# Kernel tuning notes

Measured on AMD Instinct MI355X. Metric: run time of the kernel, lower is better.

Reference implementation:

```python
import jax, jax.numpy as jnp
import numpy as np

NTIME = 20      # number of time blocks
V = 128         # vehicle_num per time block
F_OUT = 128     # out_features (== in_features here)
ALPHA = 0.2     # LeakyReLU negative slope
NEG = -9e15     # mask fill value used by the torch module


def setup_inputs() -> dict:
    key = jax.random.key(0)
    k1, k2, k3, k4 = jax.random.split(key, 4)
    h = jax.random.normal(k1, (NTIME * V, F_OUT), dtype=jnp.float32)
    # binary adjacency mask, broadcast over the feature dim like the torch code
    adj = jax.random.randint(k2, (V, V, 1), 0, 2).astype(jnp.float32)
    share_weight = jax.random.normal(k3, (F_OUT, F_OUT), dtype=jnp.float32) * 0.05
    a = jax.random.normal(k4, (2 * F_OUT, F_OUT), dtype=jnp.float32) * 0.05
    return {"h": h, "adj": adj, "share_weight": share_weight, "a": a}


def reference(h, adj, share_weight, a):
    # Wh: [N, F]
    Wh = h @ share_weight
    # a_input @ a decomposes: e[p,q,:] = leakyrelu(Wh[p] @ a[:F] + Wh[q] @ a[F:])
    # Only the block-diagonal (per-time) slices of e are ever used, so compute
    # blocks directly instead of the full NxNxF tensor.
    a1, a2 = a[:F_OUT], a[F_OUT:]
    e1 = (Wh @ a1).reshape(NTIME, V, F_OUT)  # [T, v, F]
    e2 = (Wh @ a2).reshape(NTIME, V, F_OUT)
    e = e1[:, :, None, :] + e2[:, None, :, :]           # [T, v, v, F]
    e = jnp.where(e > 0, e, ALPHA * e)                   # LeakyReLU
    masked = jnp.where(adj[None] > 0, e, NEG)            # mask per time block
    # torch softmax(dim=1) on [v, v, F] blocks -> axis=2 here (the j index)
    attention_raw = jax.nn.softmax(masked, axis=2)       # [T, v, v, F]
    # training=False => dropout is identity.
    # h_prime[t,b,f] = sum_j att[t,b,j,f] * Wh[t,j,f]  (the diagonal-of-matmul trick)
    Whb = Wh.reshape(NTIME, V, F_OUT)
    h_prime = jnp.einsum('tbjf,tjf->tbf', attention_raw, Whb)
    out = jax.nn.elu(h_prime)                            # concat=True branch
    return (out, attention_raw)
```

## Files before the change

kernel.cpp:

```cpp
#include <hip/hip_runtime.h>
#include <hip/hip_bf16.h>
#include <math.h>

#define NTIME 20
#define V 128
#define F 128
constexpr float ALPHA = 0.2f;

__global__ __launch_bounds__(128) void k_wa(const float* __restrict__ W,
                                            const float* __restrict__ a,
                                            float* __restrict__ Wa) {
  const int i = blockIdx.x;
  const int s = blockIdx.y;
  const int k = threadIdx.x;
  __shared__ float wrow[F];
  wrow[k] = W[i * F + k];
  __syncthreads();
  const float* as = a + s * F * F;
  float acc = 0.f;
#pragma unroll 8
  for (int m = 0; m < F; ++m) acc += wrow[m] * as[m * F + k];
  Wa[(s * F + i) * F + k] = acc;
}

__global__ __launch_bounds__(256) void k_gemm(const float* __restrict__ h,
                                              const float* __restrict__ W,
                                              const float* __restrict__ Wa,
                                              float* __restrict__ Wh,
                                              float* __restrict__ E1,
                                              float* __restrict__ E2) {
  __shared__ float Alds[64][129];
  __shared__ float Blds[128][64];
  const int tid = threadIdx.x;
  const int rb = blockIdx.x * 64;
  const int matc = blockIdx.y >> 1;
  const int cb = (blockIdx.y & 1) * 64;

#pragma unroll
  for (int p = 0; p < 8; ++p) {
    int id = tid + p * 256;
    int row = id >> 5;
    int c0 = (id & 31) * 4;
    float4 v = *reinterpret_cast<const float4*>(&h[(rb + row) * F + c0]);
    Alds[row][c0 + 0] = v.x; Alds[row][c0 + 1] = v.y;
    Alds[row][c0 + 2] = v.z; Alds[row][c0 + 3] = v.w;
  }
  const float* src = (matc == 0) ? W : (Wa + (matc - 1) * F * F);
#pragma unroll
  for (int p = 0; p < 8; ++p) {
    int id = tid + p * 256;
    int k = id >> 4;
    int c0 = (id & 15) * 4;
    float4 v = *reinterpret_cast<const float4*>(&src[k * F + cb + c0]);
    Blds[k][c0 + 0] = v.x; Blds[k][c0 + 1] = v.y;
    Blds[k][c0 + 2] = v.z; Blds[k][c0 + 3] = v.w;
  }
  __syncthreads();

  const int tx = tid & 15;
  const int ty = tid >> 4;
  float acc[4][4] = {};
#pragma unroll 4
  for (int k = 0; k < 128; ++k) {
    float4 bv = *reinterpret_cast<const float4*>(&Blds[k][tx * 4]);
    float a0 = Alds[ty * 4 + 0][k];
    float a1 = Alds[ty * 4 + 1][k];
    float a2 = Alds[ty * 4 + 2][k];
    float a3 = Alds[ty * 4 + 3][k];
    acc[0][0] += a0 * bv.x; acc[0][1] += a0 * bv.y; acc[0][2] += a0 * bv.z; acc[0][3] += a0 * bv.w;
    acc[1][0] += a1 * bv.x; acc[1][1] += a1 * bv.y; acc[1][2] += a1 * bv.z; acc[1][3] += a1 * bv.w;
    acc[2][0] += a2 * bv.x; acc[2][1] += a2 * bv.y; acc[2][2] += a2 * bv.z; acc[2][3] += a2 * bv.w;
    acc[3][0] += a3 * bv.x; acc[3][1] += a3 * bv.y; acc[3][2] += a3 * bv.z; acc[3][3] += a3 * bv.w;
  }

  float* Dp = (matc == 0) ? Wh : ((matc == 1) ? E1 : E2);
  const int gr0 = rb + ty * 4;
  const int c0 = cb + tx * 4;
#pragma unroll
  for (int i = 0; i < 4; ++i) {
    float4 v;
    v.x = acc[i][0]; v.y = acc[i][1]; v.z = acc[i][2]; v.w = acc[i][3];
    *reinterpret_cast<float4*>(&Dp[(gr0 + i) * F + c0]) = v;
  }
}

__global__ __launch_bounds__(256) void k_attn(const float* __restrict__ Wh,
                                              const float* __restrict__ E1,
                                              const float* __restrict__ E2,
                                              const float* __restrict__ adj,
                                              float* __restrict__ out,
                                              float* __restrict__ att) {
  __shared__ float sA[4][F];
  __shared__ float hA[4][F];
  __shared__ float invA[F];

  const int r = blockIdx.x;
  const int t = r >> 7;
  const int b = r & 127;
  const int w = threadIdx.x >> 6;
  const int lane = threadIdx.x & 63;
  const int fc = lane * 2;
  const int j0 = w * 32;

  const float* E2t = E2 + t * V * F;
  const float* Wht = Wh + t * V * F;
  const float* adjb = adj + b * V;
  const float2 e1v = *reinterpret_cast<const float2*>(E1 + r * F + fc);

  float s0 = 0.f, s1 = 0.f, h0 = 0.f, h1 = 0.f;
#pragma unroll 4
  for (int jj = 0; jj < 32; ++jj) {
    const int j = j0 + jj;
    if (adjb[j] > 0.f) {
      float2 e2 = *reinterpret_cast<const float2*>(E2t + j * F + fc);
      float x0 = e1v.x + e2.x, x1 = e1v.y + e2.y;
      x0 = x0 > 0.f ? x0 : ALPHA * x0;
      x1 = x1 > 0.f ? x1 : ALPHA * x1;
      float p0 = __expf(x0), p1 = __expf(x1);
      float2 wv = *reinterpret_cast<const float2*>(Wht + j * F + fc);
      s0 += p0; s1 += p1;
      h0 += p0 * wv.x; h1 += p1 * wv.y;
    }
  }
  sA[w][fc] = s0; sA[w][fc + 1] = s1;
  hA[w][fc] = h0; hA[w][fc + 1] = h1;
  __syncthreads();

  const float S0 = sA[0][fc] + sA[1][fc] + sA[2][fc] + sA[3][fc];
  const float S1 = sA[0][fc + 1] + sA[1][fc + 1] + sA[2][fc + 1] + sA[3][fc + 1];
  const bool uni = (S0 == 0.f);
  const float inv0 = uni ? (1.f / (float)V) : (1.f / S0);
  const float inv1 = uni ? (1.f / (float)V) : (1.f / S1);
  if (w == 0) { invA[fc] = inv0; invA[fc + 1] = inv1; }

  if (w == 0) {
    float H0, H1;
    if (uni) {
      H0 = 0.f; H1 = 0.f;
      for (int j = 0; j < V; ++j) {
        float2 wv = *reinterpret_cast<const float2*>(Wht + j * F + fc);
        H0 += wv.x; H1 += wv.y;
      }
      H0 *= inv0; H1 *= inv1;
    } else {
      H0 = (hA[0][fc] + hA[1][fc] + hA[2][fc] + hA[3][fc]) * inv0;
      H1 = (hA[0][fc + 1] + hA[1][fc + 1] + hA[2][fc + 1] + hA[3][fc + 1]) * inv1;
    }
    float2 ov;
    ov.x = H0 > 0.f ? H0 : __expf(H0) - 1.f;
    ov.y = H1 > 0.f ? H1 : __expf(H1) - 1.f;
    *reinterpret_cast<float2*>(out + r * F + fc) = ov;
  }
  __syncthreads();

  const int jh = lane >> 5;
  const int f4 = (lane & 31) * 4;
  const float4 e1q = *reinterpret_cast<const float4*>(E1 + r * F + f4);
  const float4 invq = *reinterpret_cast<const float4*>(&invA[f4]);
  float* attb = att + (size_t)r * (V * F);

#pragma unroll 4
  for (int jj = 0; jj < 16; ++jj) {
    const int j = j0 + jj * 2 + jh;
    const float av = adjb[j];
    const float4 e2q = *reinterpret_cast<const float4*>(E2t + j * F + f4);
    float x0 = e1q.x + e2q.x, x1 = e1q.y + e2q.y;
    float x2 = e1q.z + e2q.z, x3 = e1q.w + e2q.w;
    x0 = x0 > 0.f ? x0 : ALPHA * x0;
    x1 = x1 > 0.f ? x1 : ALPHA * x1;
    x2 = x2 > 0.f ? x2 : ALPHA * x2;
    x3 = x3 > 0.f ? x3 : ALPHA * x3;
    float4 o;
    o.x = __expf(x0) * invq.x;
    o.y = __expf(x1) * invq.y;
    o.z = __expf(x2) * invq.z;
    o.w = __expf(x3) * invq.w;
    if (uni) {
      o.x = invq.x; o.y = invq.y; o.z = invq.z; o.w = invq.w;
    } else if (av <= 0.f) {
      o.x = 0.f; o.y = 0.f; o.z = 0.f; o.w = 0.f;
    }
    *reinterpret_cast<float4*>(attb + j * F + f4) = o;
  }
}

extern "C" void kernel_launch(void* const* d_in, const int* in_sizes, int n_in,
                              void* d_out, int out_size, void* d_ws, size_t ws_size,
                              hipStream_t stream) {
  (void)in_sizes; (void)n_in; (void)out_size; (void)ws_size;
  const float* h   = (const float*)d_in[0];
  const float* adj = (const float*)d_in[1];
  const float* W   = (const float*)d_in[2];
  const float* a   = (const float*)d_in[3];

  float* Wh = (float*)d_ws;
  float* E1 = Wh + NTIME * V * F;
  float* E2 = E1 + NTIME * V * F;
  float* Wa = E2 + NTIME * V * F;

  float* out = (float*)d_out;
  float* att = out + NTIME * V * F;

  k_wa<<<dim3(128, 2), 128, 0, stream>>>(W, a, Wa);
  k_gemm<<<dim3(40, 6), 256, 0, stream>>>(h, W, Wa, Wh, E1, E2);
  k_attn<<<dim3(NTIME * V), 256, 0, stream>>>(Wh, E1, E2, adj, out, att);
}
```

Measured before the change: 210.3 us.

## Split attention kernel into reduction pass and flat grid-stride attention writer

The fused attention kernel is split in two. The first kernel computes the softmax sums, writes out, and stores the per-row inverse sums and a uniform flag to workspace. The second kernel writes the attention tensor through a flat, fully coalesced index over all elements. This is meant to make the dominant attention store bandwidth-bound with better parallelism. In exchange it adds a kernel launch, an extra workspace round-trip for INV/UNI, and recomputes exp for masked entries.

```diff
diff --git a/kernel.cpp b/kernel.cpp
--- a/kernel.cpp
+++ b/kernel.cpp
@@ -84,15 +84,15 @@
   }
 }
 
-__global__ __launch_bounds__(256) void k_attn(const float* __restrict__ Wh,
-                                              const float* __restrict__ E1,
-                                              const float* __restrict__ E2,
-                                              const float* __restrict__ adj,
-                                              float* __restrict__ out,
-                                              float* __restrict__ att) {
+__global__ __launch_bounds__(256) void k_attn_a(const float* __restrict__ Wh,
+                                                const float* __restrict__ E1,
+                                                const float* __restrict__ E2,
+                                                const float* __restrict__ adj,
+                                                float* __restrict__ out,
+                                                float* __restrict__ INV,
+                                                float* __restrict__ UNI) {
   __shared__ float sA[4][F];
   __shared__ float hA[4][F];
-  __shared__ float invA[F];
 
   const int r = blockIdx.x;
   const int t = r >> 7;
@@ -126,14 +126,16 @@
   hA[w][fc] = h0; hA[w][fc + 1] = h1;
   __syncthreads();
 
-  const float S0 = sA[0][fc] + sA[1][fc] + sA[2][fc] + sA[3][fc];
-  const float S1 = sA[0][fc + 1] + sA[1][fc + 1] + sA[2][fc + 1] + sA[3][fc + 1];
-  const bool uni = (S0 == 0.f);
-  const float inv0 = uni ? (1.f / (float)V) : (1.f / S0);
-  const float inv1 = uni ? (1.f / (float)V) : (1.f / S1);
-  if (w == 0) { invA[fc] = inv0; invA[fc + 1] = inv1; }
-
   if (w == 0) {
+    const float S0 = sA[0][fc] + sA[1][fc] + sA[2][fc] + sA[3][fc];
+    const float S1 = sA[0][fc + 1] + sA[1][fc + 1] + sA[2][fc + 1] + sA[3][fc + 1];
+    const bool uni = (S0 == 0.f);
+    const float inv0 = uni ? (1.f / (float)V) : (1.f / S0);
+    const float inv1 = uni ? (1.f / (float)V) : (1.f / S1);
+    float2 iv; iv.x = inv0; iv.y = inv1;
+    *reinterpret_cast<float2*>(INV + r * F + fc) = iv;
+    if (threadIdx.x == 0) UNI[r] = uni ? 1.f : 0.f;
+
     float H0, H1;
     if (uni) {
       H0 = 0.f; H1 = 0.f;
@@ -151,36 +153,45 @@
     ov.y = H1 > 0.f ? H1 : __expf(H1) - 1.f;
     *reinterpret_cast<float2*>(out + r * F + fc) = ov;
   }
-  __syncthreads();
-
-  const int jh = lane >> 5;
-  const int f4 = (lane & 31) * 4;
-  const float4 e1q = *reinterpret_cast<const float4*>(E1 + r * F + f4);
-  const float4 invq = *reinterpret_cast<const float4*>(&invA[f4]);
-  float* attb = att + (size_t)r * (V * F);
-
+}
+
+__global__ __launch_bounds__(256) void k_attn_b(const float* __restrict__ E1,
+                                                const float* __restrict__ E2,
+                                                const float* __restrict__ adj,
+                                                const float* __restrict__ INV,
+                                                const float* __restrict__ UNI,
+                                                float* __restrict__ att) {
+  const int gidx = blockIdx.x * 256 + threadIdx.x;
 #pragma unroll 4
-  for (int jj = 0; jj < 16; ++jj) {
-    const int j = j0 + jj * 2 + jh;
-    const float av = adjb[j];
-    const float4 e2q = *reinterpret_cast<const float4*>(E2t + j * F + f4);
+  for (int it = 0; it < 16; ++it) {
+    const int idx = gidx + it * 655360;
+    const int elems = idx << 2;
+    const int f0 = elems & 127;
+    const int j = (elems >> 7) & 127;
+    const int r = elems >> 14;
+    const int b = r & 127;
+    const int t = r >> 7;
+
+    const float4 e1q = *reinterpret_cast<const float4*>(E1 + r * F + f0);
+    const float4 invq = *reinterpret_cast<const float4*>(INV + r * F + f0);
+    const float4 e2q = *reinterpret_cast<const float4*>(E2 + (t * V + j) * F + f0);
+    const float av = adj[b * V + j];
+    const float u = UNI[r];
+
     float x0 = e1q.x + e2q.x, x1 = e1q.y + e2q.y;
     float x2 = e1q.z + e2q.z, x3 = e1q.w + e2q.w;
     x0 = x0 > 0.f ? x0 : ALPHA * x0;
     x1 = x1 > 0.f ? x1 : ALPHA * x1;
     x2 = x2 > 0.f ? x2 : ALPHA * x2;
     x3 = x3 > 0.f ? x3 : ALPHA * x3;
+    const float g = (av > 0.f) ? 1.f : 0.f;
     float4 o;
-    o.x = __expf(x0) * invq.x;
-    o.y = __expf(x1) * invq.y;
-    o.z = __expf(x2) * invq.z;
-    o.w = __expf(x3) * invq.w;
-    if (uni) {
-      o.x = invq.x; o.y = invq.y; o.z = invq.z; o.w = invq.w;
-    } else if (av <= 0.f) {
-      o.x = 0.f; o.y = 0.f; o.z = 0.f; o.w = 0.f;
-    }
-    *reinterpret_cast<float4*>(attb + j * F + f4) = o;
+    o.x = __expf(x0) * invq.x * g;
+    o.y = __expf(x1) * invq.y * g;
+    o.z = __expf(x2) * invq.z * g;
+    o.w = __expf(x3) * invq.w * g;
+    if (u != 0.f) { o.x = invq.x; o.y = invq.y; o.z = invq.z; o.w = invq.w; }
+    *reinterpret_cast<float4*>(att + elems) = o;
   }
 }
 
@@ -193,15 +204,18 @@
   const float* W   = (const float*)d_in[2];
   const float* a   = (const float*)d_in[3];
 
-  float* Wh = (float*)d_ws;
-  float* E1 = Wh + NTIME * V * F;
-  float* E2 = E1 + NTIME * V * F;
-  float* Wa = E2 + NTIME * V * F;
+  float* Wh  = (float*)d_ws;
+  float* E1  = Wh + NTIME * V * F;
+  float* E2  = E1 + NTIME * V * F;
+  float* Wa  = E2 + NTIME * V * F;
+  float* INV = Wa + 2 * F * F;
+  float* UNI = INV + NTIME * V * F;
 
   float* out = (float*)d_out;
   float* att = out + NTIME * V * F;
 
   k_wa<<<dim3(128, 2), 128, 0, stream>>>(W, a, Wa);
   k_gemm<<<dim3(40, 6), 256, 0, stream>>>(h, W, Wa, Wh, E1, E2);
-  k_attn<<<dim3(NTIME * V), 256, 0, stream>>>(Wh, E1, E2, adj, out, att);
-}
+  k_attn_a<<<dim3(NTIME * V), 256, 0, stream>>>(Wh, E1, E2, adj, out, INV, UNI);
+  k_attn_b<<<dim3(2560), 256, 0, stream>>>(E1, E2, adj, INV, UNI, att);
+}
```

Measured after the change: 218.2 us. 1.04x slower.
